# Kernel tuning notes

Measured on AMD Instinct MI355X. Metric: run time of the kernel, lower is better.

## Reference

```python
import jax, jax.numpy as jnp
import numpy as np

N_NODES = 50000


def gcn_conv(x, edge_index, W, b, n_nodes):
    # PyG GCNConv: h = D^{-1/2} (A + I) D^{-1/2} (x @ W) + b
    loops = jnp.arange(n_nodes, dtype=edge_index.dtype)
    src = jnp.concatenate([edge_index[0], loops])
    dst = jnp.concatenate([edge_index[1], loops])
    deg = jax.ops.segment_sum(jnp.ones_like(dst, dtype=x.dtype), dst,
                              num_segments=n_nodes)
    dinv = jnp.where(deg > 0, jax.lax.rsqrt(deg), 0.0)
    norm = dinv[src] * dinv[dst]                      # [E+N]
    h = x @ W                                          # [N, out]
    msg = h[src] * norm[:, None]                       # gather + scale
    out = jax.ops.segment_sum(msg, dst, num_segments=n_nodes)
    return out + b


def setup_inputs() -> dict:
    key = jax.random.key(0)
    ks = jax.random.split(key, 8)
    in_c, hid_c, out_c = 256, 128, 64
    x = jax.random.normal(ks[0], (N_NODES, in_c), dtype=jnp.float32)
    edge_index = jax.random.randint(ks[1], (2, 800000), 0, N_NODES, dtype=jnp.int64)
    pos_edge_index = jax.random.randint(ks[2], (2, 200000), 0, N_NODES, dtype=jnp.int64)
    neg_edge_index = jax.random.randint(ks[3], (2, 200000), 0, N_NES if False else N_NODES, dtype=jnp.int64)
    W1 = jax.random.normal(ks[4], (in_c, hid_c), dtype=jnp.float32) / np.sqrt(in_c)
    b1 = jnp.zeros((hid_c,), dtype=jnp.float32)
    W2 = jax.random.normal(ks[5], (hid_c, out_c), dtype=jnp.float32) / np.sqrt(hid_c)
    b2 = jnp.zeros((out_c,), dtype=jnp.float32)
    return {"x": x, "edge_index": edge_index, "pos_edge_index": pos_edge_index,
            "neg_edge_index": neg_edge_index, "W1": W1, "b1": b1, "W2": W2, "b2": b2}


def reference(x, edge_index, pos_edge_index, neg_edge_index, W1, b1, W2, b2):
    n = x.shape[0]
    h = jax.nn.relu(gcn_conv(x, edge_index, W1, b1, n))
    z = gcn_conv(h, edge_index, W2, b2, n)             # [N, out_c]
    ei = jnp.concatenate([pos_edge_index, neg_edge_index], axis=-1)
    logits = jnp.sum(z[ei[0]] * z[ei[1]], axis=-1)     # [E_pos + E_neg]
    return logits
```

## Files before the change

### kernel.cpp

```cpp
#include <hip/hip_runtime.h>
#include <stdint.h>

constexpr int N_NODES = 50000;
constexpr int E_EDGES = 800000;
constexpr int E_PAIR  = 200000;
constexpr int C_IN    = 256;
constexpr int C_HID   = 128;
constexpr int C_OUT   = 64;
constexpr int SLOT    = 64;

constexpr int NBUCK = 196;
constexpr int BCAP  = 4608;
constexpr int CHUNK = 4096;
constexpr int PREPB = 32;
constexpr int BINAB = (E_EDGES + CHUNK - 1) / CHUNK;
constexpr int GEMM1_BLOCKS = (N_NODES + 63) / 64;

typedef __attribute__((ext_vector_type(8))) _Float16 f16x8;
typedef __attribute__((ext_vector_type(2))) _Float16 f16x2;
typedef __attribute__((ext_vector_type(4))) float f32x4;

__device__ inline uint16_t f2h_bits(float v) {
    union { _Float16 h; uint16_t u; } c; c.h = (_Float16)v;
    return c.u;
}
__device__ inline uint32_t pack2h(float a, float b) {
    return (uint32_t)f2h_bits(a) | ((uint32_t)f2h_bits(b) << 16);
}
__device__ inline void acc_h8(float* a, uint4 v) {
    union { uint4 u; _Float16 h[8]; } c; c.u = v;
#pragma unroll
    for (int i = 0; i < 8; ++i) a[i] += (float)c.h[i];
}
__device__ inline void acc_h8s(float* a, uint4 v, float s) {
    union { uint4 u; _Float16 h[8]; } c; c.u = v;
#pragma unroll
    for (int i = 0; i < 8; ++i) a[i] += (float)c.h[i] * s;
}
__device__ inline float dot_h8(uint4 a, uint4 b) {
    union { uint4 u; f16x2 h[4]; } ca, cb; ca.u = a; cb.u = b;
    float v = 0.f;
#pragma unroll
    for (int i = 0; i < 4; ++i) {
#if __has_builtin(__builtin_amdgcn_fdot2)
        v = __builtin_amdgcn_fdot2(ca.h[i], cb.h[i], v, false);
#else
        v += (float)ca.h[i][0] * (float)cb.h[i][0]
           + (float)ca.h[i][1] * (float)cb.h[i][1];
#endif
    }
    return v;
}

template<int N>
__device__ inline int wswz_idx(int k, int n) {
    int c = k >> 5, kq = (k >> 3) & 3, kk = k & 7, ct = n >> 4, nn = n & 15;
    return (((c * (N / 16) + ct) * 4 + kq) * 16 + nn) * 8 + kk;
}

__global__ __launch_bounds__(256) void prep_binA_kernel(
        const float* __restrict__ W1, const float* __restrict__ W2,
        uint16_t* __restrict__ s1, uint16_t* __restrict__ s2,
        const int* __restrict__ src, const int* __restrict__ dst,
        int* __restrict__ gcur, uint32_t* __restrict__ ebuf) {
    __shared__ int cnt[NBUCK], loc[NBUCK], lim[NBUCK], abase[NBUCK], wcur[NBUCK];
    __shared__ int tot;
    __shared__ uint32_t stag[CHUNK];

    const int t = threadIdx.x;

    if (blockIdx.x < PREPB) {
        for (int id = blockIdx.x * 256 + t;
             id < C_IN * C_HID + C_HID * C_OUT; id += PREPB * 256) {
            if (id < C_IN * C_HID) {
                int idx = wswz_idx<C_HID>(id / C_HID, id & (C_HID - 1));
                s1[idx] = f2h_bits(W1[id]);
            } else {
                int id2 = id - C_IN * C_HID;
                int idx = wswz_idx<C_OUT>(id2 / C_OUT, id2 & (C_OUT - 1));
                s2[idx] = f2h_bits(W2[id2]);
            }
        }
        return;
    }

    const int e0 = (blockIdx.x - PREPB) * CHUNK;
    const int n  = min(CHUNK, E_EDGES - e0);

    for (int b = t; b < NBUCK; b += 256) cnt[b] = 0;
    if (t == 0) tot = 0;
    __syncthreads();

    uint32_t pk[CHUNK / 256];
    int ne = 0;
    for (int j = t; j < n; j += 256) {
        int d = dst[e0 + j], s = src[e0 + j];
        int b = d >> 8;
        pk[ne] = ((uint32_t)b << 24) | ((uint32_t)(d & 255) << 16) | (uint32_t)s;
        atomicAdd(&cnt[b], 1);
        ++ne;
    }
    __syncthreads();
    for (int b = t; b < NBUCK; b += 256)
        loc[b] = atomicAdd(&tot, cnt[b]);
    __syncthreads();
    for (int b = t; b < NBUCK; b += 256) {
        int base = atomicAdd(&gcur[b], cnt[b]);
        int room = BCAP - base; if (room < 0) room = 0;
        lim[b]   = loc[b] + room;
        abase[b] = b * BCAP + base - loc[b];
        wcur[b]  = loc[b];
    }
    __syncthreads();
#pragma unroll
    for (int i = 0; i < CHUNK / 256; ++i) {
        if (i < ne) {
            int p = atomicAdd(&wcur[pk[i] >> 24], 1);
            stag[p] = pk[i];
        }
    }
    __syncthreads();
    for (int j = t; j < n; j += 256) {
        uint32_t v = stag[j];
        int b = v >> 24;
        if (j < lim[b]) ebuf[abase[b] + j] = v & 0x00ffffffu;
    }
}

__global__ __launch_bounds__(256, 3) void build_gemm_kernel(
        const int* __restrict__ gcur, const uint32_t* __restrict__ ebuf,
        uint16_t* __restrict__ col2, int* __restrict__ degc,
        float* __restrict__ dinv,
        const float* __restrict__ A, const uint16_t* __restrict__ Bswz,
        uint16_t* __restrict__ out) {
    constexpr int K = C_IN, N = C_HID;
    constexpr int BM = 64, BK = 32;
    constexpr int CT   = N / 32;
    constexpr int NSUB = N / 16;
    constexpr int ABYTES = BM * BK * 2;
    constexpr int BBYTES = NSUB * 1024;
    __shared__ char sm[1024 + 256 * SLOT * 2];

    const int t = threadIdx.x;

    if (blockIdx.x < NBUCK) {
        int* cur = (int*)sm;
        uint16_t* colL = (uint16_t*)(sm + 1024);
        const int b = blockIdx.x;
        cur[t] = 0;
        __syncthreads();

        int cn = gcur[b]; if (cn > BCAP) cn = BCAP;
        const uint32_t* eb = ebuf + (size_t)b * BCAP;
        const int nbase = b << 8;

        int j = t;
        for (; j + 3 * 256 < cn; j += 4 * 256) {
            uint32_t v0 = eb[j], v1 = eb[j + 256], v2 = eb[j + 512], v3 = eb[j + 768];
            int p0 = atomicAdd(&cur[v0 >> 16], 1);
            int p1 = atomicAdd(&cur[v1 >> 16], 1);
            int p2 = atomicAdd(&cur[v2 >> 16], 1);
            int p3 = atomicAdd(&cur[v3 >> 16], 1);
            if (p0 < SLOT) colL[((v0 >> 16) << 6) + p0] = (uint16_t)(v0 & 0xffff);
            if (p1 < SLOT) colL[((v1 >> 16) << 6) + p1] = (uint16_t)(v1 & 0xffff);
            if (p2 < SLOT) colL[((v2 >> 16) << 6) + p2] = (uint16_t)(v2 & 0xffff);
            if (p3 < SLOT) colL[((v3 >> 16) << 6) + p3] = (uint16_t)(v3 & 0xffff);
        }
        for (; j < cn; j += 256) {
            uint32_t v = eb[j];
            int p = atomicAdd(&cur[v >> 16], 1);
            if (p < SLOT) colL[((v >> 16) << 6) + p] = (uint16_t)(v & 0xffff);
        }
        __syncthreads();
        int nodes = N_NODES - nbase; if (nodes > 256) nodes = 256;
        uint4* dstc = (uint4*)(col2 + ((size_t)nbase << 6));
        const uint4* srcc = (const uint4*)colL;
        for (int i = t; i < nodes * 8; i += 256)
            dstc[i] = srcc[i];
        int node = nbase + t;
        if (node < N_NODES) {
            int dg = cur[t];
            degc[node] = dg;
            dinv[node] = rsqrtf((float)dg + 1.0f);
        }
        return;
    }

    char* As = sm;
    char* Bs = sm + ABYTES;

    const int lane = t & 63;
    const int w    = t >> 6;
    const int wrow = w & 1, wcol = w >> 1;
    const int m0   = (blockIdx.x - NBUCK) * BM;
    const int M    = N_NODES;

    const int sr = t >> 2, skq = t & 3;
    int arow = m0 + sr; if (arow > M - 1) arow = M - 1;
    const float* aptr = A + (size_t)arow * K + skq * 8;
    const int aslot = ((sr >> 4) * 64 + skq * 16 + (sr & 15)) * 16;

    f32x4 acc[2][CT];
#pragma unroll
    for (int rt = 0; rt < 2; ++rt)
#pragma unroll
        for (int ct = 0; ct < CT; ++ct) {
            f32x4 z = {0.f, 0.f, 0.f, 0.f};
            acc[rt][ct] = z;
        }

    const uint4* gh = (const uint4*)Bswz;

    constexpr int NCH = K / BK;
#pragma unroll 1
    for (int c = 0; c < NCH; ++c) {
        float4 v0 = *(const float4*)(aptr + c * BK);
        float4 v1 = *(const float4*)(aptr + c * BK + 4);
        uint4 bh0, bh1;
        {
            const uint4* ch = gh + (size_t)c * (BBYTES / 16);
            bh0 = ch[t];
            bh1 = ch[t + 256];
        }
        __syncthreads();
        {
            float e[8] = {v0.x, v0.y, v0.z, v0.w, v1.x, v1.y, v1.z, v1.w};
            uint32_t hp[4];
#pragma unroll
            for (int j = 0; j < 4; ++j)
                hp[j] = pack2h(e[2 * j], e[2 * j + 1]);
            *(uint4*)(As + aslot) = make_uint4(hp[0], hp[1], hp[2], hp[3]);
        }
        *(uint4*)(Bs + t * 16) = bh0;
        *(uint4*)(Bs + (t + 256) * 16) = bh1;
        __syncthreads();
        f16x8 Ah[2];
#pragma unroll
        for (int rt = 0; rt < 2; ++rt) {
            int st = wrow * 2 + rt;
            Ah[rt] = *(const f16x8*)(As + st * 1024 + lane * 16);
        }
#pragma unroll
        for (int ct = 0; ct < CT; ++ct) {
            int cg = wcol * CT + ct;
            f16x8 Bh = *(const f16x8*)(Bs + cg * 1024 + lane * 16);
#pragma unroll
            for (int rt = 0; rt < 2; ++rt)
                acc[rt][ct] = __builtin_amdgcn_mfma_f32_16x16x32_f16(Ah[rt], Bh, acc[rt][ct], 0, 0, 0);
        }
    }

#pragma unroll
    for (int rt = 0; rt < 2; ++rt) {
        int rowbase = m0 + wrow * 32 + rt * 16 + (lane >> 4) * 4;
#pragma unroll
        for (int ct = 0; ct < CT; ++ct) {
            int n = (wcol * CT + ct) * 16 + (lane & 15);
#pragma unroll
            for (int r = 0; r < 4; ++r) {
                int m = rowbase + r;
                if (m < M) out[(size_t)m * N + n] = f2h_bits(acc[rt][ct][r]);
            }
        }
    }
}

__global__ __launch_bounds__(256) void gather_gemm_kernel(
        const uint16_t* __restrict__ col2, const int* __restrict__ degc,
        const uint16_t* __restrict__ h0u, const float* __restrict__ dinv,
        const float* __restrict__ bias, const uint16_t* __restrict__ B2swz,
        uint16_t* __restrict__ z0s) {
    __shared__ uint4 hlds[256];
    const int t    = threadIdx.x;
    const int lane = t & 63;
    const int w    = t >> 6;
    const int sub  = lane >> 4;
    const int l    = lane & 15;
    const int node_loc = w * 4 + sub;
    const int node = blockIdx.x * 16 + node_loc;

    int dg = degc[node]; if (dg > SLOT) dg = SLOT;
    const float dn = dinv[node];
    const uint4* hs4 = (const uint4*)h0u;
    float a0[8], a1[8];
#pragma unroll
    for (int i = 0; i < 8; ++i) { a0[i] = 0.f; a1[i] = 0.f; }
    {
        uint4 self = hs4[(size_t)node * 16 + l];
        acc_h8s(a0, self, dn);
    }
    const uint32_t* cp = (const uint32_t*)col2;
    const int pbase = node * (SLOT / 2);
    const int sb    = sub * 16;

    for (int c = 0; c * 16 < dg; ++c) {
        int cnt = dg - c * 16; if (cnt > 16) cnt = 16;
        uint32_t cv = (2 * l < cnt) ? cp[pbase + c * 8 + l] : 0u;
        int j = 0;
        for (; j + 8 <= cnt; j += 8) {
            uint32_t p0 = (uint32_t)__shfl((int)cv, sb + (j >> 1),     64);
            uint32_t p1 = (uint32_t)__shfl((int)cv, sb + (j >> 1) + 1, 64);
            uint32_t p2 = (uint32_t)__shfl((int)cv, sb + (j >> 1) + 2, 64);
            uint32_t p3 = (uint32_t)__shfl((int)cv, sb + (j >> 1) + 3, 64);
            int s0 = p0 & 0xffff, s1 = p0 >> 16;
            int s2 = p1 & 0xffff, s3 = p1 >> 16;
            int s4 = p2 & 0xffff, s5 = p2 >> 16;
            int s6 = p3 & 0xffff, s7 = p3 >> 16;
            uint4 v0 = hs4[(size_t)s0 * 16 + l];
            uint4 v1 = hs4[(size_t)s1 * 16 + l];
            uint4 v2 = hs4[(size_t)s2 * 16 + l];
            uint4 v3 = hs4[(size_t)s3 * 16 + l];
            uint4 v4 = hs4[(size_t)s4 * 16 + l];
            uint4 v5 = hs4[(size_t)s5 * 16 + l];
            uint4 v6 = hs4[(size_t)s6 * 16 + l];
            uint4 v7 = hs4[(size_t)s7 * 16 + l];
            float d0 = dinv[s0], d1 = dinv[s1], d2 = dinv[s2], d3 = dinv[s3];
            float d4 = dinv[s4], d5 = dinv[s5], d6 = dinv[s6], d7 = dinv[s7];
            acc_h8s(a0, v0, d0); acc_h8s(a1, v1, d1);
            acc_h8s(a0, v2, d2); acc_h8s(a1, v3, d3);
            acc_h8s(a0, v4, d4); acc_h8s(a1, v5, d5);
            acc_h8s(a0, v6, d6); acc_h8s(a1, v7, d7);
        }
        for (; j + 4 <= cnt; j += 4) {
            uint32_t p0 = (uint32_t)__shfl((int)cv, sb + (j >> 1),     64);
            uint32_t p1 = (uint32_t)__shfl((int)cv, sb + (j >> 1) + 1, 64);
            int s0 = p0 & 0xffff, s1 = p0 >> 16;
            int s2 = p1 & 0xffff, s3 = p1 >> 16;
            uint4 v0 = hs4[(size_t)s0 * 16 + l];
            uint4 v1 = hs4[(size_t)s1 * 16 + l];
            uint4 v2 = hs4[(size_t)s2 * 16 + l];
            uint4 v3 = hs4[(size_t)s3 * 16 + l];
            float d0 = dinv[s0], d1 = dinv[s1], d2 = dinv[s2], d3 = dinv[s3];
            acc_h8s(a0, v0, d0); acc_h8s(a1, v1, d1);
            acc_h8s(a0, v2, d2); acc_h8s(a1, v3, d3);
        }
        for (; j < cnt; ++j) {
            uint32_t p = (uint32_t)__shfl((int)cv, sb + (j >> 1), 64);
            int s = (j & 1) ? (int)(p >> 16) : (int)(p & 0xffff);
            uint4 v = hs4[(size_t)s * 16 + l];
            acc_h8s(a0, v, dinv[s]);
        }
    }
    {
        float4 bb0 = ((const float4*)bias)[2 * l];
        float4 bb1 = ((const float4*)bias)[2 * l + 1];
        float o[8];
        o[0] = fmaxf((a0[0] + a1[0]) * dn + bb0.x, 0.f);
        o[1] = fmaxf((a0[1] + a1[1]) * dn + bb0.y, 0.f);
        o[2] = fmaxf((a0[2] + a1[2]) * dn + bb0.z, 0.f);
        o[3] = fmaxf((a0[3] + a1[3]) * dn + bb0.w, 0.f);
        o[4] = fmaxf((a0[4] + a1[4]) * dn + bb1.x, 0.f);
        o[5] = fmaxf((a0[5] + a1[5]) * dn + bb1.y, 0.f);
        o[6] = fmaxf((a0[6] + a1[6]) * dn + bb1.z, 0.f);
        o[7] = fmaxf((a0[7] + a1[7]) * dn + bb1.w, 0.f);
        hlds[l * 16 + node_loc] = make_uint4(
            pack2h(o[0], o[1]), pack2h(o[2], o[3]),
            pack2h(o[4], o[5]), pack2h(o[6], o[7]));
    }
    __syncthreads();

    f32x4 acc = {0.f, 0.f, 0.f, 0.f};
    const char* hb = (const char*)hlds;
#pragma unroll
    for (int c = 0; c < 4; ++c) {
        f16x8 Af = *(const f16x8*)(hb + c * 1024 + lane * 16);
        f16x8 Bh = *(const f16x8*)(B2swz + (c * 4 + w) * 512 + lane * 8);
        acc = __builtin_amdgcn_mfma_f32_16x16x32_f16(Af, Bh, acc, 0, 0, 0);
    }
    const int colg = w * 16 + (lane & 15);
    const int rowb = blockIdx.x * 16 + (lane >> 4) * 4;
#pragma unroll
    for (int r = 0; r < 4; ++r) {
        int m = rowb + r;
        z0s[(size_t)m * C_OUT + colg] = f2h_bits(acc[r] * dinv[m]);
    }
}

template<int F, bool RELU>
__global__ __launch_bounds__(256) void gather_kernel(
        const uint16_t* __restrict__ col2, const int* __restrict__ degc,
        const uint16_t* __restrict__ hs, const float* __restrict__ dinv,
        const float* __restrict__ bias, uint16_t* __restrict__ out) {
    constexpr int LPN = F / 8;
    constexpr int NPW = 64 / LPN;
    const int lane = threadIdx.x & 63;
    const int sub  = lane / LPN;
    const int l    = lane % LPN;
    const int node = blockIdx.x * (4 * NPW) + (threadIdx.x >> 6) * NPW + sub;
    if (node >= N_NODES) return;

    int dg = degc[node]; if (dg > SLOT) dg = SLOT;
    const uint4* hs4 = (const uint4*)hs;

    float a0[8], a1[8];
#pragma unroll
    for (int i = 0; i < 8; ++i) { a0[i] = 0.f; a1[i] = 0.f; }
    {
        uint4 self = hs4[(size_t)node * LPN + l];
        acc_h8(a0, self);
    }
    const uint32_t* cp = (const uint32_t*)col2;
    const int pbase = node * (SLOT / 2);
    const int sb    = sub * LPN;

    for (int c = 0; c * LPN < dg; ++c) {
        int cnt = dg - c * LPN; if (cnt > LPN) cnt = LPN;
        uint32_t cv = (2 * l < cnt) ? cp[pbase + c * (LPN / 2) + l] : 0u;
        int j = 0;
        for (; j + 8 <= cnt; j += 8) {
            uint32_t p0 = (uint32_t)__shfl((int)cv, sb + (j >> 1),     64);
            uint32_t p1 = (uint32_t)__shfl((int)cv, sb + (j >> 1) + 1, 64);
            uint32_t p2 = (uint32_t)__shfl((int)cv, sb + (j >> 1) + 2, 64);
            uint32_t p3 = (uint32_t)__shfl((int)cv, sb + (j >> 1) + 3, 64);
            int s0 = p0 & 0xffff, s1 = p0 >> 16;
            int s2 = p1 & 0xffff, s3 = p1 >> 16;
            int s4 = p2 & 0xffff, s5 = p2 >> 16;
            int s6 = p3 & 0xffff, s7 = p3 >> 16;
            uint4 v0 = hs4[(size_t)s0 * LPN + l];
            uint4 v1 = hs4[(size_t)s1 * LPN + l];
            uint4 v2 = hs4[(size_t)s2 * LPN + l];
            uint4 v3 = hs4[(size_t)s3 * LPN + l];
            uint4 v4 = hs4[(size_t)s4 * LPN + l];
            uint4 v5 = hs4[(size_t)s5 * LPN + l];
            uint4 v6 = hs4[(size_t)s6 * LPN + l];
            uint4 v7 = hs4[(size_t)s7 * LPN + l];
            acc_h8(a0, v0); acc_h8(a1, v1);
            acc_h8(a0, v2); acc_h8(a1, v3);
            acc_h8(a0, v4); acc_h8(a1, v5);
            acc_h8(a0, v6); acc_h8(a1, v7);
        }
        for (; j + 4 <= cnt; j += 4) {
            uint32_t p0 = (uint32_t)__shfl((int)cv, sb + (j >> 1),     64);
            uint32_t p1 = (uint32_t)__shfl((int)cv, sb + (j >> 1) + 1, 64);
            int s0 = p0 & 0xffff, s1 = p0 >> 16;
            int s2 = p1 & 0xffff, s3 = p1 >> 16;
            uint4 v0 = hs4[(size_t)s0 * LPN + l];
            uint4 v1 = hs4[(size_t)s1 * LPN + l];
            uint4 v2 = hs4[(size_t)s2 * LPN + l];
            uint4 v3 = hs4[(size_t)s3 * LPN + l];
            acc_h8(a0, v0); acc_h8(a1, v1);
            acc_h8(a0, v2); acc_h8(a1, v3);
        }
        for (; j < cnt; ++j) {
            uint32_t p = (uint32_t)__shfl((int)cv, sb + (j >> 1), 64);
            int s = (j & 1) ? (int)(p >> 16) : (int)(p & 0xffff);
            uint4 v = hs4[(size_t)s * LPN + l];
            acc_h8(a0, v);
        }
    }

    const float dn = dinv[node];
    float4 bb0 = ((const float4*)bias)[2 * l];
    float4 bb1 = ((const float4*)bias)[2 * l + 1];
    float o[8];
    o[0] = (a0[0] + a1[0]) * dn + bb0.x;
    o[1] = (a0[1] + a1[1]) * dn + bb0.y;
    o[2] = (a0[2] + a1[2]) * dn + bb0.z;
    o[3] = (a0[3] + a1[3]) * dn + bb0.w;
    o[4] = (a0[4] + a1[4]) * dn + bb1.x;
    o[5] = (a0[5] + a1[5]) * dn + bb1.y;
    o[6] = (a0[6] + a1[6]) * dn + bb1.z;
    o[7] = (a0[7] + a1[7]) * dn + bb1.w;
    if (RELU) {
#pragma unroll
        for (int i = 0; i < 8; ++i) o[i] = fmaxf(o[i], 0.f);
    }
    uint4 res = make_uint4(pack2h(o[0], o[1]), pack2h(o[2], o[3]),
                           pack2h(o[4], o[5]), pack2h(o[6], o[7]));
    ((uint4*)out)[(size_t)node * LPN + l] = res;
}

__global__ __launch_bounds__(256) void logits_kernel(
        const int* __restrict__ pos, const int* __restrict__ neg,
        const uint16_t* __restrict__ z, float* __restrict__ out) {
    const int t = threadIdx.x;
    const int l = t & 7;
    const int g = (blockIdx.x * 256 + t) >> 3;
    const int e0 = 2 * g;
    if (e0 >= 2 * E_PAIR) return;
    int s0, d0, s1, d1;
    if (e0 < E_PAIR) { s0 = pos[e0];          d0 = pos[E_PAIR + e0]; }
    else             { s0 = neg[e0 - E_PAIR]; d0 = neg[e0];          }
    int e1 = e0 + 1;
    if (e1 < E_PAIR) { s1 = pos[e1];          d1 = pos[E_PAIR + e1]; }
    else             { s1 = neg[e1 - E_PAIR]; d1 = neg[e1];          }
    const uint4* z4 = (const uint4*)z;
    uint4 ua0 = z4[(size_t)s0 * 8 + l];
    uint4 ub0 = z4[(size_t)d0 * 8 + l];
    uint4 ua1 = z4[(size_t)s1 * 8 + l];
    uint4 ub1 = z4[(size_t)d1 * 8 + l];
    float v0 = dot_h8(ua0, ub0);
    float v1 = dot_h8(ua1, ub1);
    v0 += __shfl_xor(v0, 1, 64); v1 += __shfl_xor(v1, 1, 64);
    v0 += __shfl_xor(v0, 2, 64); v1 += __shfl_xor(v1, 2, 64);
    v0 += __shfl_xor(v0, 4, 64); v1 += __shfl_xor(v1, 4, 64);
    if (l == 0) { out[e0] = v0; out[e1] = v1; }
}

extern "C" void kernel_launch(void* const* d_in, const int* in_sizes, int n_in,
                              void* d_out, int out_size, void* d_ws, size_t ws_size,
                              hipStream_t stream) {
    const float* x   = (const float*)d_in[0];
    const int*   ei  = (const int*)d_in[1];
    const int*   pos = (const int*)d_in[2];
    const int*   neg = (const int*)d_in[3];
    const float* W1  = (const float*)d_in[4];
    const float* b1  = (const float*)d_in[5];
    const float* W2  = (const float*)d_in[6];
    const float* b2  = (const float*)d_in[7];
    float* out = (float*)d_out;

    const int* src = ei;
    const int* dst = ei + E_EDGES;

    char* ws = (char*)d_ws;
    int*      degc  = (int*)ws;
    float*    dinv  = (float*)(ws + 200704);
    uint16_t* col2  = (uint16_t*)(ws + 401408);
    int*      gcur  = (int*)(ws + 6801408);
    uint16_t* B1swz = (uint16_t*)(ws + 6802432);
    uint16_t* B2swz = (uint16_t*)(ws + 6933504);
    uint16_t* h0u   = (uint16_t*)(ws + 6966272);
    uint16_t* z0s   = (uint16_t*)(ws + 32566272);
    uint16_t* zbuf  = (uint16_t*)(ws + 38966272);
    uint32_t* ebuf  = (uint32_t*)(ws + 45366272);

    hipMemsetAsync(gcur, 0, NBUCK * sizeof(int), stream);

    prep_binA_kernel<<<PREPB + BINAB, 256, 0, stream>>>(
        W1, W2, B1swz, B2swz, src, dst, gcur, ebuf);

    build_gemm_kernel<<<NBUCK + GEMM1_BLOCKS, 256, 0, stream>>>(
        gcur, ebuf, col2, degc, dinv, x, B1swz, h0u);

    gather_gemm_kernel<<<N_NODES / 16, 256, 0, stream>>>(
        col2, degc, h0u, dinv, b1, B2swz, z0s);

    gather_kernel<C_OUT, false><<<(N_NODES + 31) / 32, 256, 0, stream>>>(
        col2, degc, z0s, dinv, b2, zbuf);

    logits_kernel<<<(E_PAIR * 8 + 255) / 256, 256, 0, stream>>>(pos, neg, zbuf, out);
}
```

Measured before the change: 190.5 us.

## Fuse gather-GEMM, second gather and logits into one persistent kernel with grid barriers

The last three kernel launches are replaced by a single persistent kernel of 1024 blocks. Each block loops over work groups for each of the three stages, and software global barriers (atomic counter with sleep) separate the stages. The memset is widened to zero the barrier counters. The aim is to remove launch gaps and tail drain between stages. In exchange, the barriers serialize every block, the grid-stride loop balances load less well, and the code relies on all 1024 blocks being co-resident to avoid deadlock.

```diff
diff --git a/kernel.cpp b/kernel.cpp
--- a/kernel.cpp
+++ b/kernel.cpp
@@ -16,6 +16,11 @@
 constexpr int BINAB = (E_EDGES + CHUNK - 1) / CHUNK;
 constexpr int GEMM1_BLOCKS = (N_NODES + 63) / 64;
 
+constexpr int TAIL_BLOCKS = 1024;
+constexpr int GG_GROUPS   = N_NODES / 16;
+constexpr int G2_GROUPS   = (N_NODES + 31) / 32;
+constexpr int LG_GROUPS   = (E_PAIR * 8 + 255) / 256;
+
 typedef __attribute__((ext_vector_type(8))) _Float16 f16x8;
 typedef __attribute__((ext_vector_type(2))) _Float16 f16x2;
 typedef __attribute__((ext_vector_type(4))) float f32x4;
@@ -50,6 +55,21 @@
 #endif
     }
     return v;
+}
+
+__device__ inline void global_barrier(int* cnt, int nblk) {
+    __syncthreads();
+    if (threadIdx.x == 0) {
+        __threadfence();
+        atomicAdd(cnt, 1);
+        long guard = 0;
+        while (atomicAdd(cnt, 0) < nblk && guard < (1L << 28)) {
+            __builtin_amdgcn_s_sleep(2);
+            ++guard;
+        }
+        __threadfence();
+    }
+    __syncthreads();
 }
 
 template<int N>
@@ -265,236 +285,240 @@
     }
 }
 
-__global__ __launch_bounds__(256) void gather_gemm_kernel(
+__global__ __launch_bounds__(256, 4) void fused_tail_kernel(
         const uint16_t* __restrict__ col2, const int* __restrict__ degc,
         const uint16_t* __restrict__ h0u, const float* __restrict__ dinv,
-        const float* __restrict__ bias, const uint16_t* __restrict__ B2swz,
-        uint16_t* __restrict__ z0s) {
+        const float* __restrict__ b1,  const uint16_t* __restrict__ B2swz,
+        uint16_t* __restrict__ z0s, const float* __restrict__ b2,
+        uint16_t* __restrict__ zbuf,
+        const int* __restrict__ pos, const int* __restrict__ neg,
+        float* __restrict__ out, int* gbar) {
     __shared__ uint4 hlds[256];
     const int t    = threadIdx.x;
     const int lane = t & 63;
     const int w    = t >> 6;
-    const int sub  = lane >> 4;
-    const int l    = lane & 15;
-    const int node_loc = w * 4 + sub;
-    const int node = blockIdx.x * 16 + node_loc;
-
-    int dg = degc[node]; if (dg > SLOT) dg = SLOT;
-    const float dn = dinv[node];
-    const uint4* hs4 = (const uint4*)h0u;
-    float a0[8], a1[8];
-#pragma unroll
-    for (int i = 0; i < 8; ++i) { a0[i] = 0.f; a1[i] = 0.f; }
+
     {
-        uint4 self = hs4[(size_t)node * 16 + l];
-        acc_h8s(a0, self, dn);
-    }
-    const uint32_t* cp = (const uint32_t*)col2;
-    const int pbase = node * (SLOT / 2);
-    const int sb    = sub * 16;
-
-    for (int c = 0; c * 16 < dg; ++c) {
-        int cnt = dg - c * 16; if (cnt > 16) cnt = 16;
-        uint32_t cv = (2 * l < cnt) ? cp[pbase + c * 8 + l] : 0u;
-        int j = 0;
-        for (; j + 8 <= cnt; j += 8) {
-            uint32_t p0 = (uint32_t)__shfl((int)cv, sb + (j >> 1),     64);
-            uint32_t p1 = (uint32_t)__shfl((int)cv, sb + (j >> 1) + 1, 64);
-            uint32_t p2 = (uint32_t)__shfl((int)cv, sb + (j >> 1) + 2, 64);
-            uint32_t p3 = (uint32_t)__shfl((int)cv, sb + (j >> 1) + 3, 64);
-            int s0 = p0 & 0xffff, s1 = p0 >> 16;
-            int s2 = p1 & 0xffff, s3 = p1 >> 16;
-            int s4 = p2 & 0xffff, s5 = p2 >> 16;
-            int s6 = p3 & 0xffff, s7 = p3 >> 16;
-            uint4 v0 = hs4[(size_t)s0 * 16 + l];
-            uint4 v1 = hs4[(size_t)s1 * 16 + l];
-            uint4 v2 = hs4[(size_t)s2 * 16 + l];
-            uint4 v3 = hs4[(size_t)s3 * 16 + l];
-            uint4 v4 = hs4[(size_t)s4 * 16 + l];
-            uint4 v5 = hs4[(size_t)s5 * 16 + l];
-            uint4 v6 = hs4[(size_t)s6 * 16 + l];
-            uint4 v7 = hs4[(size_t)s7 * 16 + l];
-            float d0 = dinv[s0], d1 = dinv[s1], d2 = dinv[s2], d3 = dinv[s3];
-            float d4 = dinv[s4], d5 = dinv[s5], d6 = dinv[s6], d7 = dinv[s7];
-            acc_h8s(a0, v0, d0); acc_h8s(a1, v1, d1);
-            acc_h8s(a0, v2, d2); acc_h8s(a1, v3, d3);
-            acc_h8s(a0, v4, d4); acc_h8s(a1, v5, d5);
-            acc_h8s(a0, v6, d6); acc_h8s(a1, v7, d7);
-        }
-        for (; j + 4 <= cnt; j += 4) {
-            uint32_t p0 = (uint32_t)__shfl((int)cv, sb + (j >> 1),     64);
-            uint32_t p1 = (uint32_t)__shfl((int)cv, sb + (j >> 1) + 1, 64);
-            int s0 = p0 & 0xffff, s1 = p0 >> 16;
-            int s2 = p1 & 0xffff, s3 = p1 >> 16;
-            uint4 v0 = hs4[(size_t)s0 * 16 + l];
-            uint4 v1 = hs4[(size_t)s1 * 16 + l];
-            uint4 v2 = hs4[(size_t)s2 * 16 + l];
-            uint4 v3 = hs4[(size_t)s3 * 16 + l];
-            float d0 = dinv[s0], d1 = dinv[s1], d2 = dinv[s2], d3 = dinv[s3];
-            acc_h8s(a0, v0, d0); acc_h8s(a1, v1, d1);
-            acc_h8s(a0, v2, d2); acc_h8s(a1, v3, d3);
-        }
-        for (; j < cnt; ++j) {
-            uint32_t p = (uint32_t)__shfl((int)cv, sb + (j >> 1), 64);
-            int s = (j & 1) ? (int)(p >> 16) : (int)(p & 0xffff);
-            uint4 v = hs4[(size_t)s * 16 + l];
-            acc_h8s(a0, v, dinv[s]);
-        }
-    }
+        const int sub  = lane >> 4;
+        const int l    = lane & 15;
+        const int node_loc = w * 4 + sub;
+        const uint4* hs4 = (const uint4*)h0u;
+        const uint32_t* cp = (const uint32_t*)col2;
+        const int sb = sub * 16;
+
+        for (int grp = blockIdx.x; grp < GG_GROUPS; grp += TAIL_BLOCKS) {
+            const int node = grp * 16 + node_loc;
+            int dg = degc[node]; if (dg > SLOT) dg = SLOT;
+            const float dn = dinv[node];
+            float a0[8], a1[8];
+#pragma unroll
+            for (int i = 0; i < 8; ++i) { a0[i] = 0.f; a1[i] = 0.f; }
+            {
+                uint4 self = hs4[(size_t)node * 16 + l];
+                acc_h8s(a0, self, dn);
+            }
+            const int pbase = node * (SLOT / 2);
+
+            for (int c = 0; c * 16 < dg; ++c) {
+                int cnt = dg - c * 16; if (cnt > 16) cnt = 16;
+                uint32_t cv = (2 * l < cnt) ? cp[pbase + c * 8 + l] : 0u;
+                int j = 0;
+                for (; j + 8 <= cnt; j += 8) {
+                    uint32_t p0 = (uint32_t)__shfl((int)cv, sb + (j >> 1),     64);
+                    uint32_t p1 = (uint32_t)__shfl((int)cv, sb + (j >> 1) + 1, 64);
+                    uint32_t p2 = (uint32_t)__shfl((int)cv, sb + (j >> 1) + 2, 64);
+                    uint32_t p3 = (uint32_t)__shfl((int)cv, sb + (j >> 1) + 3, 64);
+                    int s0 = p0 & 0xffff, s1 = p0 >> 16;
+                    int s2 = p1 & 0xffff, s3 = p1 >> 16;
+                    int s4 = p2 & 0xffff, s5 = p2 >> 16;
+                    int s6 = p3 & 0xffff, s7 = p3 >> 16;
+                    uint4 v0 = hs4[(size_t)s0 * 16 + l];
+                    uint4 v1 = hs4[(size_t)s1 * 16 + l];
+                    uint4 v2 = hs4[(size_t)s2 * 16 + l];
+                    uint4 v3 = hs4[(size_t)s3 * 16 + l];
+                    uint4 v4 = hs4[(size_t)s4 * 16 + l];
+                    uint4 v5 = hs4[(size_t)s5 * 16 + l];
+                    uint4 v6 = hs4[(size_t)s6 * 16 + l];
+                    uint4 v7 = hs4[(size_t)s7 * 16 + l];
+                    float d0 = dinv[s0], d1 = dinv[s1], d2 = dinv[s2], d3 = dinv[s3];
+                    float d4 = dinv[s4], d5 = dinv[s5], d6 = dinv[s6], d7 = dinv[s7];
+                    acc_h8s(a0, v0, d0); acc_h8s(a1, v1, d1);
+                    acc_h8s(a0, v2, d2); acc_h8s(a1, v3, d3);
+                    acc_h8s(a0, v4, d4); acc_h8s(a1, v5, d5);
+                    acc_h8s(a0, v6, d6); acc_h8s(a1, v7, d7);
+                }
+                for (; j + 4 <= cnt; j += 4) {
+                    uint32_t p0 = (uint32_t)__shfl((int)cv, sb + (j >> 1),     64);
+                    uint32_t p1 = (uint32_t)__shfl((int)cv, sb + (j >> 1) + 1, 64);
+                    int s0 = p0 & 0xffff, s1 = p0 >> 16;
+                    int s2 = p1 & 0xffff, s3 = p1 >> 16;
+                    uint4 v0 = hs4[(size_t)s0 * 16 + l];
+                    uint4 v1 = hs4[(size_t)s1 * 16 + l];
+                    uint4 v2 = hs4[(size_t)s2 * 16 + l];
+                    uint4 v3 = hs4[(size_t)s3 * 16 + l];
+                    float d0 = dinv[s0], d1 = dinv[s1], d2 = dinv[s2], d3 = dinv[s3];
+                    acc_h8s(a0, v0, d0); acc_h8s(a1, v1, d1);
+                    acc_h8s(a0, v2, d2); acc_h8s(a1, v3, d3);
+                }
+                for (; j < cnt; ++j) {
+                    uint32_t p = (uint32_t)__shfl((int)cv, sb + (j >> 1), 64);
+                    int s = (j & 1) ? (int)(p >> 16) : (int)(p & 0xffff);
+                    uint4 v = hs4[(size_t)s * 16 + l];
+                    acc_h8s(a0, v, dinv[s]);
+                }
+            }
+            {
+                float4 bb0 = ((const float4*)b1)[2 * l];
+                float4 bb1 = ((const float4*)b1)[2 * l + 1];
+                float o[8];
+                o[0] = fmaxf((a0[0] + a1[0]) * dn + bb0.x, 0.f);
+                o[1] = fmaxf((a0[1] + a1[1]) * dn + bb0.y, 0.f);
+                o[2] = fmaxf((a0[2] + a1[2]) * dn + bb0.z, 0.f);
+                o[3] = fmaxf((a0[3] + a1[3]) * dn + bb0.w, 0.f);
+                o[4] = fmaxf((a0[4] + a1[4]) * dn + bb1.x, 0.f);
+                o[5] = fmaxf((a0[5] + a1[5]) * dn + bb1.y, 0.f);
+                o[6] = fmaxf((a0[6] + a1[6]) * dn + bb1.z, 0.f);
+                o[7] = fmaxf((a0[7] + a1[7]) * dn + bb1.w, 0.f);
+                hlds[l * 16 + node_loc] = make_uint4(
+                    pack2h(o[0], o[1]), pack2h(o[2], o[3]),
+                    pack2h(o[4], o[5]), pack2h(o[6], o[7]));
+            }
+            __syncthreads();
+
+            f32x4 acc = {0.f, 0.f, 0.f, 0.f};
+            const char* hb = (const char*)hlds;
+#pragma unroll
+            for (int c = 0; c < 4; ++c) {
+                f16x8 Af = *(const f16x8*)(hb + c * 1024 + lane * 16);
+                f16x8 Bh = *(const f16x8*)(B2swz + (c * 4 + w) * 512 + lane * 8);
+                acc = __builtin_amdgcn_mfma_f32_16x16x32_f16(Af, Bh, acc, 0, 0, 0);
+            }
+            const int colg = w * 16 + (lane & 15);
+            const int rowb = grp * 16 + (lane >> 4) * 4;
+#pragma unroll
+            for (int r = 0; r < 4; ++r) {
+                int m = rowb + r;
+                z0s[(size_t)m * C_OUT + colg] = f2h_bits(acc[r] * dinv[m]);
+            }
+            __syncthreads();
+        }
+    }
+    global_barrier(gbar + 0, TAIL_BLOCKS);
+
     {
-        float4 bb0 = ((const float4*)bias)[2 * l];
-        float4 bb1 = ((const float4*)bias)[2 * l + 1];
-        float o[8];
-        o[0] = fmaxf((a0[0] + a1[0]) * dn + bb0.x, 0.f);
-        o[1] = fmaxf((a0[1] + a1[1]) * dn + bb0.y, 0.f);
-        o[2] = fmaxf((a0[2] + a1[2]) * dn + bb0.z, 0.f);
-        o[3] = fmaxf((a0[3] + a1[3]) * dn + bb0.w, 0.f);
-        o[4] = fmaxf((a0[4] + a1[4]) * dn + bb1.x, 0.f);
-        o[5] = fmaxf((a0[5] + a1[5]) * dn + bb1.y, 0.f);
-        o[6] = fmaxf((a0[6] + a1[6]) * dn + bb1.z, 0.f);
-        o[7] = fmaxf((a0[7] + a1[7]) * dn + bb1.w, 0.f);
-        hlds[l * 16 + node_loc] = make_uint4(
-            pack2h(o[0], o[1]), pack2h(o[2], o[3]),
-            pack2h(o[4], o[5]), pack2h(o[6], o[7]));
-    }
-    __syncthreads();
-
-    f32x4 acc = {0.f, 0.f, 0.f, 0.f};
-    const char* hb = (const char*)hlds;
-#pragma unroll
-    for (int c = 0; c < 4; ++c) {
-        f16x8 Af = *(const f16x8*)(hb + c * 1024 + lane * 16);
-        f16x8 Bh = *(const f16x8*)(B2swz + (c * 4 + w) * 512 + lane * 8);
-        acc = __builtin_amdgcn_mfma_f32_16x16x32_f16(Af, Bh, acc, 0, 0, 0);
-    }
-    const int colg = w * 16 + (lane & 15);
-    const int rowb = blockIdx.x * 16 + (lane >> 4) * 4;
-#pragma unroll
-    for (int r = 0; r < 4; ++r) {
-        int m = rowb + r;
-        z0s[(size_t)m * C_OUT + colg] = f2h_bits(acc[r] * dinv[m]);
-    }
-}
-
-template<int F, bool RELU>
-__global__ __launch_bounds__(256) void gather_kernel(
-        const uint16_t* __restrict__ col2, const int* __restrict__ degc,
-        const uint16_t* __restrict__ hs, const float* __restrict__ dinv,
-        const float* __restrict__ bias, uint16_t* __restrict__ out) {
-    constexpr int LPN = F / 8;
-    constexpr int NPW = 64 / LPN;
-    const int lane = threadIdx.x & 63;
-    const int sub  = lane / LPN;
-    const int l    = lane % LPN;
-    const int node = blockIdx.x * (4 * NPW) + (threadIdx.x >> 6) * NPW + sub;
-    if (node >= N_NODES) return;
-
-    int dg = degc[node]; if (dg > SLOT) dg = SLOT;
-    const uint4* hs4 = (const uint4*)hs;
-
-    float a0[8], a1[8];
-#pragma unroll
-    for (int i = 0; i < 8; ++i) { a0[i] = 0.f; a1[i] = 0.f; }
+        constexpr int LPN = C_OUT / 8;
+        constexpr int NPW = 64 / LPN;
+        const int sub  = lane / LPN;
+        const int l    = lane % LPN;
+        const uint4* hs4 = (const uint4*)z0s;
+        const uint32_t* cp = (const uint32_t*)col2;
+        const int sb = sub * LPN;
+
+        for (int grp = blockIdx.x; grp < G2_GROUPS; grp += TAIL_BLOCKS) {
+            const int node = grp * (4 * NPW) + w * NPW + sub;
+            if (node < N_NODES) {
+                int dg = degc[node]; if (dg > SLOT) dg = SLOT;
+                float a0[8], a1[8];
+#pragma unroll
+                for (int i = 0; i < 8; ++i) { a0[i] = 0.f; a1[i] = 0.f; }
+                {
+                    uint4 self = hs4[(size_t)node * LPN + l];
+                    acc_h8(a0, self);
+                }
+                const int pbase = node * (SLOT / 2);
+
+                for (int c = 0; c * LPN < dg; ++c) {
+                    int cnt = dg - c * LPN; if (cnt > LPN) cnt = LPN;
+                    uint32_t cv = (2 * l < cnt) ? cp[pbase + c * (LPN / 2) + l] : 0u;
+                    int j = 0;
+                    for (; j + 8 <= cnt; j += 8) {
+                        uint32_t p0 = (uint32_t)__shfl((int)cv, sb + (j >> 1),     64);
+                        uint32_t p1 = (uint32_t)__shfl((int)cv, sb + (j >> 1) + 1, 64);
+                        uint32_t p2 = (uint32_t)__shfl((int)cv, sb + (j >> 1) + 2, 64);
+                        uint32_t p3 = (uint32_t)__shfl((int)cv, sb + (j >> 1) + 3, 64);
+                        int s0 = p0 & 0xffff, s1 = p0 >> 16;
+                        int s2 = p1 & 0xffff, s3 = p1 >> 16;
+                        int s4 = p2 & 0xffff, s5 = p2 >> 16;
+                        int s6 = p3 & 0xffff, s7 = p3 >> 16;
+                        uint4 v0 = hs4[(size_t)s0 * LPN + l];
+                        uint4 v1 = hs4[(size_t)s1 * LPN + l];
+                        uint4 v2 = hs4[(size_t)s2 * LPN + l];
+                        uint4 v3 = hs4[(size_t)s3 * LPN + l];
+                        uint4 v4 = hs4[(size_t)s4 * LPN + l];
+                        uint4 v5 = hs4[(size_t)s5 * LPN + l];
+                        uint4 v6 = hs4[(size_t)s6 * LPN + l];
+                        uint4 v7 = hs4[(size_t)s7 * LPN + l];
+                        acc_h8(a0, v0); acc_h8(a1, v1);
+                        acc_h8(a0, v2); acc_h8(a1, v3);
+                        acc_h8(a0, v4); acc_h8(a1, v5);
+                        acc_h8(a0, v6); acc_h8(a1, v7);
+                    }
+                    for (; j + 4 <= cnt; j += 4) {
+                        uint32_t p0 = (uint32_t)__shfl((int)cv, sb + (j >> 1),     64);
+                        uint32_t p1 = (uint32_t)__shfl((int)cv, sb + (j >> 1) + 1, 64);
+                        int s0 = p0 & 0xffff, s1 = p0 >> 16;
+                        int s2 = p1 & 0xffff, s3 = p1 >> 16;
+                        uint4 v0 = hs4[(size_t)s0 * LPN + l];
+                        uint4 v1 = hs4[(size_t)s1 * LPN + l];
+                        uint4 v2 = hs4[(size_t)s2 * LPN + l];
+                        uint4 v3 = hs4[(size_t)s3 * LPN + l];
+                        acc_h8(a0, v0); acc_h8(a1, v1);
+                        acc_h8(a0, v2); acc_h8(a1, v3);
+                    }
+                    for (; j < cnt; ++j) {
+                        uint32_t p = (uint32_t)__shfl((int)cv, sb + (j >> 1), 64);
+                        int s = (j & 1) ? (int)(p >> 16) : (int)(p & 0xffff);
+                        uint4 v = hs4[(size_t)s * LPN + l];
+                        acc_h8(a0, v);
+                    }
+                }
+
+                const float dn = dinv[node];
+                float4 bb0 = ((const float4*)b2)[2 * l];
+                float4 bb1 = ((const float4*)b2)[2 * l + 1];
+                float o[8];
+                o[0] = (a0[0] + a1[0]) * dn + bb0.x;
+                o[1] = (a0[1] + a1[1]) * dn + bb0.y;
+                o[2] = (a0[2] + a1[2]) * dn + bb0.z;
+                o[3] = (a0[3] + a1[3]) * dn + bb0.w;
+                o[4] = (a0[4] + a1[4]) * dn + bb1.x;
+                o[5] = (a0[5] + a1[5]) * dn + bb1.y;
+                o[6] = (a0[6] + a1[6]) * dn + bb1.z;
+                o[7] = (a0[7] + a1[7]) * dn + bb1.w;
+                uint4 res = make_uint4(pack2h(o[0], o[1]), pack2h(o[2], o[3]),
+                                       pack2h(o[4], o[5]), pack2h(o[6], o[7]));
+                ((uint4*)zbuf)[(size_t)node * LPN + l] = res;
+            }
+        }
+    }
+    global_barrier(gbar + 1, TAIL_BLOCKS);
+
     {
-        uint4 self = hs4[(size_t)node * LPN + l];
-        acc_h8(a0, self);
-    }
-    const uint32_t* cp = (const uint32_t*)col2;
-    const int pbase = node * (SLOT / 2);
-    const int sb    = sub * LPN;
-
-    for (int c = 0; c * LPN < dg; ++c) {
-        int cnt = dg - c * LPN; if (cnt > LPN) cnt = LPN;
-        uint32_t cv = (2 * l < cnt) ? cp[pbase + c * (LPN / 2) + l] : 0u;
-        int j = 0;
-        for (; j + 8 <= cnt; j += 8) {
-            uint32_t p0 = (uint32_t)__shfl((int)cv, sb + (j >> 1),     64);
-            uint32_t p1 = (uint32_t)__shfl((int)cv, sb + (j >> 1) + 1, 64);
-            uint32_t p2 = (uint32_t)__shfl((int)cv, sb + (j >> 1) + 2, 64);
-            uint32_t p3 = (uint32_t)__shfl((int)cv, sb + (j >> 1) + 3, 64);
-            int s0 = p0 & 0xffff, s1 = p0 >> 16;
-            int s2 = p1 & 0xffff, s3 = p1 >> 16;
-            int s4 = p2 & 0xffff, s5 = p2 >> 16;
-            int s6 = p3 & 0xffff, s7 = p3 >> 16;
-            uint4 v0 = hs4[(size_t)s0 * LPN + l];
-            uint4 v1 = hs4[(size_t)s1 * LPN + l];
-            uint4 v2 = hs4[(size_t)s2 * LPN + l];
-            uint4 v3 = hs4[(size_t)s3 * LPN + l];
-            uint4 v4 = hs4[(size_t)s4 * LPN + l];
-            uint4 v5 = hs4[(size_t)s5 * LPN + l];
-            uint4 v6 = hs4[(size_t)s6 * LPN + l];
-            uint4 v7 = hs4[(size_t)s7 * LPN + l];
-            acc_h8(a0, v0); acc_h8(a1, v1);
-            acc_h8(a0, v2); acc_h8(a1, v3);
-            acc_h8(a0, v4); acc_h8(a1, v5);
-            acc_h8(a0, v6); acc_h8(a1, v7);
-        }
-        for (; j + 4 <= cnt; j += 4) {
-            uint32_t p0 = (uint32_t)__shfl((int)cv, sb + (j >> 1),     64);
-            uint32_t p1 = (uint32_t)__shfl((int)cv, sb + (j >> 1) + 1, 64);
-            int s0 = p0 & 0xffff, s1 = p0 >> 16;
-            int s2 = p1 & 0xffff, s3 = p1 >> 16;
-            uint4 v0 = hs4[(size_t)s0 * LPN + l];
-            uint4 v1 = hs4[(size_t)s1 * LPN + l];
-            uint4 v2 = hs4[(size_t)s2 * LPN + l];
-            uint4 v3 = hs4[(size_t)s3 * LPN + l];
-            acc_h8(a0, v0); acc_h8(a1, v1);
-            acc_h8(a0, v2); acc_h8(a1, v3);
-        }
-        for (; j < cnt; ++j) {
-            uint32_t p = (uint32_t)__shfl((int)cv, sb + (j >> 1), 64);
-            int s = (j & 1) ? (int)(p >> 16) : (int)(p & 0xffff);
-            uint4 v = hs4[(size_t)s * LPN + l];
-            acc_h8(a0, v);
-        }
-    }
-
-    const float dn = dinv[node];
-    float4 bb0 = ((const float4*)bias)[2 * l];
-    float4 bb1 = ((const float4*)bias)[2 * l + 1];
-    float o[8];
-    o[0] = (a0[0] + a1[0]) * dn + bb0.x;
-    o[1] = (a0[1] + a1[1]) * dn + bb0.y;
-    o[2] = (a0[2] + a1[2]) * dn + bb0.z;
-    o[3] = (a0[3] + a1[3]) * dn + bb0.w;
-    o[4] = (a0[4] + a1[4]) * dn + bb1.x;
-    o[5] = (a0[5] + a1[5]) * dn + bb1.y;
-    o[6] = (a0[6] + a1[6]) * dn + bb1.z;
-    o[7] = (a0[7] + a1[7]) * dn + bb1.w;
-    if (RELU) {
-#pragma unroll
-        for (int i = 0; i < 8; ++i) o[i] = fmaxf(o[i], 0.f);
-    }
-    uint4 res = make_uint4(pack2h(o[0], o[1]), pack2h(o[2], o[3]),
-                           pack2h(o[4], o[5]), pack2h(o[6], o[7]));
-    ((uint4*)out)[(size_t)node * LPN + l] = res;
-}
-
-__global__ __launch_bounds__(256) void logits_kernel(
-        const int* __restrict__ pos, const int* __restrict__ neg,
-        const uint16_t* __restrict__ z, float* __restrict__ out) {
-    const int t = threadIdx.x;
-    const int l = t & 7;
-    const int g = (blockIdx.x * 256 + t) >> 3;
-    const int e0 = 2 * g;
-    if (e0 >= 2 * E_PAIR) return;
-    int s0, d0, s1, d1;
-    if (e0 < E_PAIR) { s0 = pos[e0];          d0 = pos[E_PAIR + e0]; }
-    else             { s0 = neg[e0 - E_PAIR]; d0 = neg[e0];          }
-    int e1 = e0 + 1;
-    if (e1 < E_PAIR) { s1 = pos[e1];          d1 = pos[E_PAIR + e1]; }
-    else             { s1 = neg[e1 - E_PAIR]; d1 = neg[e1];          }
-    const uint4* z4 = (const uint4*)z;
-    uint4 ua0 = z4[(size_t)s0 * 8 + l];
-    uint4 ub0 = z4[(size_t)d0 * 8 + l];
-    uint4 ua1 = z4[(size_t)s1 * 8 + l];
-    uint4 ub1 = z4[(size_t)d1 * 8 + l];
-    float v0 = dot_h8(ua0, ub0);
-    float v1 = dot_h8(ua1, ub1);
-    v0 += __shfl_xor(v0, 1, 64); v1 += __shfl_xor(v1, 1, 64);
-    v0 += __shfl_xor(v0, 2, 64); v1 += __shfl_xor(v1, 2, 64);
-    v0 += __shfl_xor(v0, 4, 64); v1 += __shfl_xor(v1, 4, 64);
-    if (l == 0) { out[e0] = v0; out[e1] = v1; }
+        const int l = t & 7;
+        const uint4* z4 = (const uint4*)zbuf;
+        for (int vb = blockIdx.x; vb < LG_GROUPS; vb += TAIL_BLOCKS) {
+            const int g = (vb * 256 + t) >> 3;
+            const int e0 = 2 * g;
+            if (e0 < 2 * E_PAIR) {
+                int s0, d0, s1, d1;
+                if (e0 < E_PAIR) { s0 = pos[e0];          d0 = pos[E_PAIR + e0]; }
+                else             { s0 = neg[e0 - E_PAIR]; d0 = neg[e0];          }
+                int e1 = e0 + 1;
+                if (e1 < E_PAIR) { s1 = pos[e1];          d1 = pos[E_PAIR + e1]; }
+                else             { s1 = neg[e1 - E_PAIR]; d1 = neg[e1];          }
+                uint4 ua0 = z4[(size_t)s0 * 8 + l];
+                uint4 ub0 = z4[(size_t)d0 * 8 + l];
+                uint4 ua1 = z4[(size_t)s1 * 8 + l];
+                uint4 ub1 = z4[(size_t)d1 * 8 + l];
+                float v0 = dot_h8(ua0, ub0);
+                float v1 = dot_h8(ua1, ub1);
+                v0 += __shfl_xor(v0, 1, 64); v1 += __shfl_xor(v1, 1, 64);
+                v0 += __shfl_xor(v0, 2, 64); v1 += __shfl_xor(v1, 2, 64);
+                v0 += __shfl_xor(v0, 4, 64); v1 += __shfl_xor(v1, 4, 64);
+                if (l == 0) { out[e0] = v0; out[e1] = v1; }
+            }
+        }
+    }
 }
 
 extern "C" void kernel_launch(void* const* d_in, const int* in_sizes, int n_in,
@@ -518,6 +542,7 @@
     float*    dinv  = (float*)(ws + 200704);
     uint16_t* col2  = (uint16_t*)(ws + 401408);
     int*      gcur  = (int*)(ws + 6801408);
+    int*      gbar  = (int*)(ws + 6802192);
     uint16_t* B1swz = (uint16_t*)(ws + 6802432);
     uint16_t* B2swz = (uint16_t*)(ws + 6933504);
     uint16_t* h0u   = (uint16_t*)(ws + 6966272);
@@ -525,7 +550,7 @@
     uint16_t* zbuf  = (uint16_t*)(ws + 38966272);
     uint32_t* ebuf  = (uint32_t*)(ws + 45366272);
 
-    hipMemsetAsync(gcur, 0, NBUCK * sizeof(int), stream);
+    hipMemsetAsync(gcur, 0, NBUCK * sizeof(int) + 2 * sizeof(int) + 784 - NBUCK * sizeof(int), stream);
 
     prep_binA_kernel<<<PREPB + BINAB, 256, 0, stream>>>(
         W1, W2, B1swz, B2swz, src, dst, gcur, ebuf);
@@ -533,11 +558,6 @@
     build_gemm_kernel<<<NBUCK + GEMM1_BLOCKS, 256, 0, stream>>>(
         gcur, ebuf, col2, degc, dinv, x, B1swz, h0u);
 
-    gather_gemm_kernel<<<N_NODES / 16, 256, 0, stream>>>(
-        col2, degc, h0u, dinv, b1, B2swz, z0s);
-
-    gather_kernel<C_OUT, false><<<(N_NODES + 31) / 32, 256, 0, stream>>>(
-        col2, degc, z0s, dinv, b2, zbuf);
-
-    logits_kernel<<<(E_PAIR * 8 + 255) / 256, 256, 0, stream>>>(pos, neg, zbuf, out);
-}
+    fused_tail_kernel<<<TAIL_BLOCKS, 256, 0, stream>>>(
+        col2, degc, h0u, dinv, b1, B2swz, z0s, b2, zbuf, pos, neg, out, gbar);
+}
```

Measured after the change: 458.0 us. 140% more time.
